# Kernel tuning notes

Measured on AMD Instinct MI355X. Metric: run time of the kernel, lower is better.

The kernel has to match this reference:

```python
import jax, jax.numpy as jnp
import numpy as np

D_MODEL = 1024
HEAD_SIZE = 128
SCALE = float(np.sqrt(HEAD_SIZE))


def setup_inputs() -> dict:
    key = jax.random.key(0)
    kx, kq, kk, kv = jax.random.split(key, 4)
    B, T = 4, 4096
    x = jax.random.normal(kx, (B, T, D_MODEL), dtype=jnp.float32)
    # torch nn.Linear(d_model, head_size, bias=False) weight: [head_size, d_model]
    s = 1.0 / np.sqrt(D_MODEL)
    Wq = jax.random.uniform(kq, (HEAD_SIZE, D_MODEL), jnp.float32, -s, s)
    Wk = jax.random.uniform(kk, (HEAD_SIZE, D_MODEL), jnp.float32, -s, s)
    Wv = jax.random.uniform(kv, (HEAD_SIZE, D_MODEL), jnp.float32, -s, s)
    return {"x": x, "Wq": Wq, "Wk": Wk, "Wv": Wv}


def reference(x, Wq, Wk, Wv):
    B, T, C = x.shape
    q = jnp.einsum('btc,hc->bth', x, Wq)  # [B,T,hs]
    k = jnp.einsum('btc,hc->bth', x, Wk)
    v = jnp.einsum('btc,hc->bth', x, Wv)
    scores = jnp.einsum('bth,bsh->bts', q, k) / SCALE  # [B,T,T]
    causal = jnp.tril(jnp.ones((T, T), dtype=bool))
    scores = jnp.where(causal, scores, -jnp.inf)
    attn = jax.nn.softmax(scores, axis=-1)
    # dropout p=0.0 -> identity
    return jnp.einsum('bts,bsh->bth', attn, v)
```

## Files before the change

### kernel.cpp

```cpp
#include <hip/hip_runtime.h>


typedef __attribute__((ext_vector_type(8))) short short8;
typedef __attribute__((ext_vector_type(8))) unsigned short ushort8;
typedef __attribute__((ext_vector_type(4))) unsigned short ushort4v;
typedef __attribute__((ext_vector_type(4))) float f32x4;
typedef __attribute__((ext_vector_type(16))) float f32x16;
typedef __attribute__((ext_vector_type(4))) int int4v;
typedef unsigned int u32;
typedef unsigned short u16;

#define MFMA32(a, b, c) __builtin_amdgcn_mfma_f32_32x32x16_bf16((a), (b), (c), 0, 0, 0)
#define WAITVM0() asm volatile("s_waitcnt vmcnt(0)" ::: "memory")
#define NEG_INF (-1e30f)

#define CHUNK 10
#define PITEMS 119
#define NITEMS 476

__device__ __forceinline__ void gload16(const void* g, void* l) {
  __builtin_amdgcn_global_load_lds((const __attribute__((address_space(1))) u32*)g,
                                   (__attribute__((address_space(3))) u32*)l, 16, 0, 0);
}

__device__ __forceinline__ u16 f2bf(float f) {
  u32 u = __builtin_bit_cast(u32, f);
  u = u + 0x7FFFu + ((u >> 16) & 1u);
  return (u16)(u >> 16);
}

__device__ __forceinline__ u32 cvtpk(float lo, float hi) {
  u32 r;
  asm("v_cvt_pk_bf16_f32 %0, %1, %2" : "=v"(r) : "v"(lo), "v"(hi));
  return r;
}

__global__ __launch_bounds__(256) void wconv_kernel(const float* __restrict__ Wq,
                                                    const float* __restrict__ Wk,
                                                    const float* __restrict__ Wv,
                                                    u16* __restrict__ Wb) {
  int g = (blockIdx.x * 256 + threadIdx.x) * 8;
  const float* src;
  if (g < 131072)      src = Wq + g;
  else if (g < 262144) src = Wk + (g - 131072);
  else                 src = Wv + (g - 262144);
  float4 a = *(const float4*)src;
  float4 b = *(const float4*)(src + 4);
  ushort8 o;
  o[0] = f2bf(a.x); o[1] = f2bf(a.y); o[2] = f2bf(a.z); o[3] = f2bf(a.w);
  o[4] = f2bf(b.x); o[5] = f2bf(b.y); o[6] = f2bf(b.z); o[7] = f2bf(b.w);
  *(ushort8*)(Wb + g) = o;
}

#define QK_SCALE 0.127517446f

__global__ __launch_bounds__(512, 2) void qkv_proj_kernel(const float* __restrict__ x,
                                                          const u16* __restrict__ Wb,
                                                          u16* __restrict__ qout,
                                                          u16* __restrict__ kout,
                                                          u16* __restrict__ vtout) {
  __shared__ __align__(16) unsigned char Wlds[2][49152];
  __shared__ __align__(16) unsigned char Xlds[2][8192];
  const int tid = threadIdx.x;
  const int w = tid >> 6;
  const int l = tid & 63;
  const int h = l >> 5, n32 = l & 31;
  const int mh = w >> 2, ng = w & 3;
  const int m0 = (int)blockIdx.x * 64;

  const int xr = tid >> 3, xc = tid & 7;
  const float* xsrc = x + (size_t)(m0 + xr) * 1024 + xc * 8;
  unsigned char* const xw0 = (unsigned char*)Xlds[0] + xr * 128 + ((xc * 16) ^ ((xr & 7) << 4));
  unsigned char* const xw1 = (unsigned char*)Xlds[1] + xr * 128 + ((xc * 16) ^ ((xr & 7) << 4));

  f32x16 acc[3];
#pragma unroll
  for (int j = 0; j < 3; ++j)
#pragma unroll
    for (int r = 0; r < 16; ++r) acc[j][r] = 0.f;

#define STAGE_W(buf, ks)                                                       \
  {                                                                            \
    _Pragma("unroll") for (int c = 0; c < 6; ++c) {                            \
      int L = c * 512 + tid;                                                   \
      int row = L >> 3, chp = L & 7;                                           \
      int gch = chp ^ (row & 7);                                               \
      gload16((const char*)Wb + row * 2048 + (ks) * 128 + gch * 16,            \
              (unsigned char*)Wlds[buf] + c * 8192 + w * 1024);                \
    }                                                                          \
  }

  float4 xa = *(const float4*)(xsrc);
  float4 xb = *(const float4*)(xsrc + 4);
  STAGE_W(0, 0);

  const int am = mh * 32 + n32;
  const int asw = (am & 7) << 4;
  int cur = 0;

  for (int ks = 0; ks < 16; ++ks) {
    int4v xv;
    xv[0] = (int)cvtpk(xa.x, xa.y);
    xv[1] = (int)cvtpk(xa.z, xa.w);
    xv[2] = (int)cvtpk(xb.x, xb.y);
    xv[3] = (int)cvtpk(xb.z, xb.w);
    *(int4v*)(cur ? xw1 : xw0) = xv;
    __syncthreads();
    if (ks < 15) {
      xa = *(const float4*)(xsrc + (ks + 1) * 64);
      xb = *(const float4*)(xsrc + (ks + 1) * 64 + 4);
      STAGE_W(cur ^ 1, ks + 1);
    }
    const char* xb0 = (const char*)Xlds[cur];
    const char* wb0 = (const char*)Wlds[cur];
    __builtin_amdgcn_s_setprio(1);
#pragma unroll
    for (int k16 = 0; k16 < 4; ++k16) {
      short8 a = *(const short8*)(xb0 + am * 128 + ((k16 * 32 + h * 16) ^ asw));
#pragma unroll
      for (int j = 0; j < 3; ++j) {
        int nrow = (ng * 3 + j) * 32 + n32;
        short8 b = *(const short8*)(wb0 + nrow * 128 +
                                    ((k16 * 32 + h * 16) ^ ((nrow & 7) << 4)));
        acc[j] = MFMA32(a, b, acc[j]);
      }
    }
    __builtin_amdgcn_s_setprio(0);
    cur ^= 1;
  }
#undef STAGE_W

  const int m0e = m0 + mh * 32;
#pragma unroll
  for (int j = 0; j < 3; ++j) {
    int ti = ng * 3 + j;
    int gcol = ti * 32 + n32;
    if (ti < 4) {
#pragma unroll
      for (int r = 0; r < 16; ++r) {
        int row = m0e + (r & 3) + 8 * (r >> 2) + 4 * h;
        qout[(size_t)row * 128 + gcol] = f2bf(acc[j][r] * QK_SCALE);
      }
    } else if (ti < 8) {
#pragma unroll
      for (int r = 0; r < 16; ++r) {
        int row = m0e + (r & 3) + 8 * (r >> 2) + 4 * h;
        kout[(size_t)row * 128 + (gcol - 128)] = f2bf(acc[j][r]);
      }
    } else {
      int d = gcol - 256;
#pragma unroll
      for (int rq = 0; rq < 4; ++rq) {
        int t0 = m0e + rq * 8 + 4 * h;
        ushort4v o4;
#pragma unroll
        for (int i = 0; i < 4; ++i) o4[i] = f2bf(acc[j][rq * 4 + i]);
        *(ushort4v*)&vtout[(size_t)((t0 >> 12) * 128 + d) * 4096 + (t0 & 4095)] = o4;
      }
    }
  }
}

template <bool SPLIT>
__global__ __launch_bounds__(256, 2) void attn_kernel(const u16* __restrict__ qws,
                                                      const u16* __restrict__ kws,
                                                      const u16* __restrict__ vtws,
                                                      float* __restrict__ out,
                                                      float* __restrict__ opart,
                                                      float* __restrict__ mlpart) {
  __shared__ __align__(16) unsigned char Klds[2][16384];
  __shared__ __align__(16) unsigned char Vlds[2][16384];

  const int tid = threadIdx.x;
  const int w = tid >> 6;
  const int l = tid & 63;
  const int h = l >> 5, q32 = l & 31;

  int bi, qt, s_lo, s_hi, item;
  if constexpr (SPLIT) {
    item = (int)blockIdx.x;
    bi = item / PITEMS;
    int r = item - bi * PITEMS;
    int base = 0;
    qt = 0;
    while (true) {
      int cnt = (qt + 5) / 5;
      if (r < base + cnt) { break; }
      base += cnt;
      ++qt;
    }
    int cc = r - base;
    int nsteps = 2 * qt + 2;
    s_lo = cc * CHUNK;
    s_hi = (s_lo + CHUNK < nsteps) ? s_lo + CHUNK : nsteps;
  } else {
    item = 0;
    int tb = (int)blockIdx.x;
    bi = tb & 3;
    qt = 31 - (tb >> 2);
    s_lo = 0;
    s_hi = 2 * qt + 2;
  }

  const int q0w = qt * 128 + w * 32;
  const int qg = q0w + q32;
  const int grow = bi * 4096 + qg;
  const int ql = w * 32 + q32;

  short8 qf[8];
  const u16* qp = qws + (size_t)grow * 128 + h * 8;
#pragma unroll
  for (int ks = 0; ks < 8; ++ks) qf[ks] = *(const short8*)(qp + ks * 16);

  f32x16 ot[4];
#pragma unroll
  for (int dt = 0; dt < 4; ++dt)
#pragma unroll
    for (int r = 0; r < 16; ++r) ot[dt][r] = 0.f;
  float mreg = NEG_INF, lsum = 0.f;

  const char* kbatch = (const char*)kws + (size_t)bi * 4096 * 256;
  const char* vbatch = (const char*)vtws + (size_t)bi * 128 * 8192;

#define STAGE_KV(buf, kv0)                                                     \
  {                                                                            \
    _Pragma("unroll") for (int c = 0; c < 4; ++c) {                            \
      int L = c * 256 + tid;                                                   \
      int row = L >> 4, chp = L & 15;                                          \
      int gch = chp ^ (row & 7);                                               \
      gload16(kbatch + (size_t)((kv0) + row) * 256 + gch * 16,                 \
              (unsigned char*)Klds[buf] + c * 4096 + w * 1024);                \
    }                                                                          \
    _Pragma("unroll") for (int c = 0; c < 4; ++c) {                            \
      int L = c * 256 + tid;                                                   \
      int row = L >> 3, chp = L & 7;                                           \
      int gch = chp ^ (row & 7);                                               \
      gload16(vbatch + (size_t)row * 8192 + (size_t)(kv0) * 2 + gch * 16,      \
              (unsigned char*)Vlds[buf] + c * 4096 + w * 1024);                \
    }                                                                          \
  }

  STAGE_KV(0, s_lo * 64);
  int cur = 0;

  for (int s = s_lo; s < s_hi; ++s) {
    WAITVM0();
    __builtin_amdgcn_s_barrier();
    __builtin_amdgcn_sched_barrier(0);
    if (s + 1 < s_hi) STAGE_KV(cur ^ 1, (s + 1) * 64);
    const int kv0 = s * 64;
    const bool active = (kv0 <= q0w + 31);

    if (active) {
      f32x16 st0, st1;
#pragma unroll
      for (int r = 0; r < 16; ++r) { st0[r] = 0.f; st1[r] = 0.f; }
      const char* Kb = (const char*)Klds[cur];
      const int sw = (q32 & 7) << 4;
      __builtin_amdgcn_s_setprio(1);
#pragma unroll
      for (int ks = 0; ks < 8; ++ks) {
        int coff = ks * 32 + h * 16;
        short8 a0 = *(const short8*)(Kb + q32 * 256 + (coff ^ sw));
        st0 = MFMA32(a0, qf[ks], st0);
        short8 a1 = *(const short8*)(Kb + (32 + q32) * 256 + (coff ^ sw));
        st1 = MFMA32(a1, qf[ks], st1);
      }
      __builtin_amdgcn_s_setprio(0);

      if (kv0 + 63 > q0w) {
#pragma unroll
        for (int r = 0; r < 16; ++r) {
          int kvr = kv0 + (r & 3) + 8 * (r >> 2) + 4 * h;
          if (kvr > qg) st0[r] = NEG_INF;
          if (kvr + 32 > qg) st1[r] = NEG_INF;
        }
      }

      float tmax = st0[0];
#pragma unroll
      for (int r = 1; r < 16; ++r) tmax = fmaxf(tmax, st0[r]);
#pragma unroll
      for (int r = 0; r < 16; ++r) tmax = fmaxf(tmax, st1[r]);
      tmax = fmaxf(tmax, __shfl_xor(tmax, 32));
      if (!__all(tmax <= mreg + 8.0f)) {
        float mnew = fmaxf(mreg, tmax);
        float alpha = exp2f(mreg - mnew);
        lsum *= alpha;
#pragma unroll
        for (int dt = 0; dt < 4; ++dt)
#pragma unroll
          for (int r = 0; r < 16; ++r) ot[dt][r] *= alpha;
        mreg = mnew;
      }
      float rs = 0.f;
#pragma unroll
      for (int r = 0; r < 16; ++r) { st0[r] = exp2f(st0[r] - mreg); rs += st0[r]; }
#pragma unroll
      for (int r = 0; r < 16; ++r) { st1[r] = exp2f(st1[r] - mreg); rs += st1[r]; }
      rs += __shfl_xor(rs, 32);
      lsum += rs;

      const char* Vb = (const char*)Vlds[cur];
      __builtin_amdgcn_s_setprio(1);
#pragma unroll
      for (int t = 0; t < 4; ++t) {
        const f32x16& stt = (t < 2) ? st0 : st1;
        const int rb = (t & 1) * 8;
        u32 A0 = cvtpk(stt[rb + 0], stt[rb + 1]);
        u32 C0 = cvtpk(stt[rb + 2], stt[rb + 3]);
        u32 B0 = cvtpk(stt[rb + 4], stt[rb + 5]);
        u32 D0 = cvtpk(stt[rb + 6], stt[rb + 7]);
        u32 Ax = (u32)__shfl_xor((int)A0, 32);
        u32 Bx = (u32)__shfl_xor((int)B0, 32);
        u32 Cx = (u32)__shfl_xor((int)C0, 32);
        u32 Dx = (u32)__shfl_xor((int)D0, 32);
        int4v pbv;
        pbv[0] = (int)(h ? Bx : A0);
        pbv[1] = (int)(h ? Dx : C0);
        pbv[2] = (int)(h ? B0 : Ax);
        pbv[3] = (int)(h ? D0 : Cx);
        short8 pb = __builtin_bit_cast(short8, pbv);
#pragma unroll
        for (int dt = 0; dt < 4; ++dt) {
          int row = dt * 32 + q32;
          short8 va = *(const short8*)(Vb + row * 128 + ((t * 32 + h * 16) ^ sw));
          ot[dt] = MFMA32(va, pb, ot[dt]);
        }
      }
      __builtin_amdgcn_s_setprio(0);
    }
    cur ^= 1;
  }

  if constexpr (!SPLIT) {
    float inv = 1.0f / lsum;
    float* ob = out + (size_t)grow * 128;
#pragma unroll
    for (int dt = 0; dt < 4; ++dt)
#pragma unroll
      for (int rq = 0; rq < 4; ++rq) {
        f32x4 v4;
#pragma unroll
        for (int i = 0; i < 4; ++i) v4[i] = ot[dt][rq * 4 + i] * inv;
        *(f32x4*)(ob + dt * 32 + rq * 8 + 4 * h) = v4;
      }
  } else {
    float* ob = opart + (size_t)item * 16384 + (size_t)ql * 128;
#pragma unroll
    for (int dt = 0; dt < 4; ++dt)
#pragma unroll
      for (int rq = 0; rq < 4; ++rq) {
        f32x4 v4;
#pragma unroll
        for (int i = 0; i < 4; ++i) v4[i] = ot[dt][rq * 4 + i];
        *(f32x4*)(ob + dt * 32 + rq * 8 + 4 * h) = v4;
      }
    if (h == 0) {
      mlpart[item * 128 + ql] = mreg;
      mlpart[NITEMS * 128 + item * 128 + ql] = lsum;
    }
  }
#undef STAGE_KV
}

__global__ __launch_bounds__(256) void combine_kernel(const float* __restrict__ opart,
                                                      const float* __restrict__ mlpart,
                                                      float* __restrict__ out) {
  int idx = blockIdx.x * 256 + threadIdx.x;
  int row = idx >> 7, d = idx & 127;
  int bi = row >> 12, lrow = row & 4095;
  int qt = lrow >> 7, ql = lrow & 127;
  int base = 0;
#pragma unroll 1
  for (int j = 0; j < qt; ++j) base += (j + 5) / 5;
  int nspl = (qt + 5) / 5;
  int it0 = bi * PITEMS + base;

  float M = NEG_INF;
#pragma unroll 1
  for (int j = 0; j < nspl; ++j)
    M = fmaxf(M, mlpart[(it0 + j) * 128 + ql]);
  float L = 0.f, O = 0.f;
#pragma unroll 1
  for (int j = 0; j < nspl; ++j) {
    float s = exp2f(mlpart[(it0 + j) * 128 + ql] - M);
    L += mlpart[NITEMS * 128 + (it0 + j) * 128 + ql] * s;
    O += opart[(size_t)(it0 + j) * 16384 + (size_t)ql * 128 + d] * s;
  }
  out[(size_t)row * 128 + d] = O / L;
}

extern "C" void kernel_launch(void* const* d_in, const int* in_sizes, int n_in,
                              void* d_out, int out_size, void* d_ws, size_t ws_size,
                              hipStream_t stream) {
  (void)in_sizes; (void)n_in; (void)out_size;
  const float* x  = (const float*)d_in[0];
  const float* Wq = (const float*)d_in[1];
  const float* Wk = (const float*)d_in[2];
  const float* Wv = (const float*)d_in[3];
  float* out = (float*)d_out;
  char* ws = (char*)d_ws;
  u16* qws  = (u16*)(ws);
  u16* kws  = (u16*)(ws + (4u << 20));
  u16* vtws = (u16*)(ws + (8u << 20));
  u16* Wb   = (u16*)(ws + (12u << 20));
  float* opart  = (float*)(ws + (13u << 20));
  float* mlpart = (float*)(ws + (47u << 20));

  wconv_kernel<<<dim3(192), dim3(256), 0, stream>>>(Wq, Wk, Wv, Wb);
  qkv_proj_kernel<<<dim3(256), dim3(512), 0, stream>>>(x, Wb, qws, kws, vtws);
  if (ws_size >= ((size_t)48 << 20)) {
    attn_kernel<true><<<dim3(NITEMS), dim3(256), 0, stream>>>(qws, kws, vtws, nullptr, opart, mlpart);
    combine_kernel<<<dim3(8192), dim3(256), 0, stream>>>(opart, mlpart, out);
  } else {
    attn_kernel<false><<<dim3(128), dim3(256), 0, stream>>>(qws, kws, vtws, out, nullptr, nullptr);
  }
}
```

Measured before the change: 92.62 us.

## Retile QKV projection, triple-buffer weights, split K/V staging, and rebalance attention chunks

The QKV projection moves to 32-row tiles with 256 threads and a K-step of 32. Weights are triple-buffered, waits use partial vmcnt, and Q/K outputs are staged through LDS for coalesced 16-byte stores. The attention kernel single-buffers V and loads it in a separate phase overlapped with QK/softmax, which cuts LDS so occupancy can rise to 3 blocks per CU. It also uses smaller split chunks (8) with more work items and a strided block-to-item mapping. These changes aim to improve overlap and load balance, at the cost of extra barriers per step and more partial results for the combine pass.

```diff
diff --git a/kernel.cpp b/kernel.cpp
--- a/kernel.cpp
+++ b/kernel.cpp
@@ -7,16 +7,19 @@
 typedef __attribute__((ext_vector_type(4))) float f32x4;
 typedef __attribute__((ext_vector_type(16))) float f32x16;
 typedef __attribute__((ext_vector_type(4))) int int4v;
+typedef __attribute__((ext_vector_type(2))) unsigned int u32x2;
 typedef unsigned int u32;
 typedef unsigned short u16;
 
 #define MFMA32(a, b, c) __builtin_amdgcn_mfma_f32_32x32x16_bf16((a), (b), (c), 0, 0, 0)
-#define WAITVM0() asm volatile("s_waitcnt vmcnt(0)" ::: "memory")
+#define WAITVM(n) asm volatile("s_waitcnt vmcnt(" #n ")" ::: "memory")
+#define WAITLGKM0() asm volatile("s_waitcnt lgkmcnt(0)" ::: "memory")
+#define SCHEDB() __builtin_amdgcn_sched_barrier(0)
 #define NEG_INF (-1e30f)
 
-#define CHUNK 10
-#define PITEMS 119
-#define NITEMS 476
+#define CHUNK 8
+#define PITEMS 144
+#define NITEMS 576
 
 __device__ __forceinline__ void gload16(const void* g, void* l) {
   __builtin_amdgcn_global_load_lds((const __attribute__((address_space(1))) u32*)g,
@@ -54,24 +57,22 @@
 
 #define QK_SCALE 0.127517446f
 
-__global__ __launch_bounds__(512, 2) void qkv_proj_kernel(const float* __restrict__ x,
+__global__ __launch_bounds__(256, 2) void qkv_proj_kernel(const float* __restrict__ x,
                                                           const u16* __restrict__ Wb,
                                                           u16* __restrict__ qout,
                                                           u16* __restrict__ kout,
                                                           u16* __restrict__ vtout) {
-  __shared__ __align__(16) unsigned char Wlds[2][49152];
-  __shared__ __align__(16) unsigned char Xlds[2][8192];
+  __shared__ __align__(16) unsigned char Wlds[3][24576];
+  __shared__ __align__(16) unsigned char Xlds[2][2048];
   const int tid = threadIdx.x;
   const int w = tid >> 6;
   const int l = tid & 63;
   const int h = l >> 5, n32 = l & 31;
-  const int mh = w >> 2, ng = w & 3;
-  const int m0 = (int)blockIdx.x * 64;
+  const int m0 = (int)blockIdx.x * 32;
 
   const int xr = tid >> 3, xc = tid & 7;
-  const float* xsrc = x + (size_t)(m0 + xr) * 1024 + xc * 8;
-  unsigned char* const xw0 = (unsigned char*)Xlds[0] + xr * 128 + ((xc * 16) ^ ((xr & 7) << 4));
-  unsigned char* const xw1 = (unsigned char*)Xlds[1] + xr * 128 + ((xc * 16) ^ ((xr & 7) << 4));
+  const float* xsrc = x + (size_t)(m0 + xr) * 1024 + xc * 4;
+  const int xbyte = ((((xc >> 1) ^ (xr & 3)) << 4) | ((xc & 1) << 3));
 
   f32x16 acc[3];
 #pragma unroll
@@ -82,76 +83,75 @@
 #define STAGE_W(buf, ks)                                                       \
   {                                                                            \
     _Pragma("unroll") for (int c = 0; c < 6; ++c) {                            \
-      int L = c * 512 + tid;                                                   \
-      int row = L >> 3, chp = L & 7;                                           \
-      int gch = chp ^ (row & 7);                                               \
-      gload16((const char*)Wb + row * 2048 + (ks) * 128 + gch * 16,            \
-              (unsigned char*)Wlds[buf] + c * 8192 + w * 1024);                \
+      int L = c * 256 + tid;                                                   \
+      int row = L >> 2, chp = L & 3;                                           \
+      int gch = chp ^ (row & 3);                                               \
+      gload16((const char*)Wb + row * 2048 + (ks) * 64 + gch * 16,             \
+              (unsigned char*)Wlds[buf] + c * 4096 + w * 1024);                \
     }                                                                          \
   }
+#define WRITE_X(buf, v4)                                                       \
+  {                                                                            \
+    u32x2 p;                                                                   \
+    p[0] = cvtpk((v4).x, (v4).y);                                              \
+    p[1] = cvtpk((v4).z, (v4).w);                                              \
+    *(u32x2*)((unsigned char*)Xlds[buf] + xr * 64 + xbyte) = p;                \
+  }
 
   float4 xa = *(const float4*)(xsrc);
-  float4 xb = *(const float4*)(xsrc + 4);
   STAGE_W(0, 0);
-
-  const int am = mh * 32 + n32;
-  const int asw = (am & 7) << 4;
-  int cur = 0;
-
-  for (int ks = 0; ks < 16; ++ks) {
-    int4v xv;
-    xv[0] = (int)cvtpk(xa.x, xa.y);
-    xv[1] = (int)cvtpk(xa.z, xa.w);
-    xv[2] = (int)cvtpk(xb.x, xb.y);
-    xv[3] = (int)cvtpk(xb.z, xb.w);
-    *(int4v*)(cur ? xw1 : xw0) = xv;
-    __syncthreads();
-    if (ks < 15) {
-      xa = *(const float4*)(xsrc + (ks + 1) * 64);
-      xb = *(const float4*)(xsrc + (ks + 1) * 64 + 4);
-      STAGE_W(cur ^ 1, ks + 1);
-    }
-    const char* xb0 = (const char*)Xlds[cur];
-    const char* wb0 = (const char*)Wlds[cur];
+  float4 xb = *(const float4*)(xsrc + 32);
+  STAGE_W(1, 1);
+  WRITE_X(0, xa);
+
+  for (int s = 0; s < 32; ++s) {
+    if (s < 31) { WAITVM(7); } else { WAITVM(0); }
+    WAITLGKM0();
+    __builtin_amdgcn_s_barrier();
+    SCHEDB();
+    if (s < 31) WRITE_X((s + 1) & 1, xb);
+    if (s < 30) {
+      xb = *(const float4*)(xsrc + (s + 2) * 32);
+      STAGE_W((s + 2) % 3, s + 2);
+    }
+    SCHEDB();
+    const char* xb0 = (const char*)Xlds[s & 1];
+    const char* wb0 = (const char*)Wlds[s % 3];
     __builtin_amdgcn_s_setprio(1);
 #pragma unroll
-    for (int k16 = 0; k16 < 4; ++k16) {
-      short8 a = *(const short8*)(xb0 + am * 128 + ((k16 * 32 + h * 16) ^ asw));
+    for (int k16 = 0; k16 < 2; ++k16) {
+      short8 a = *(const short8*)(xb0 + n32 * 64 +
+                                  ((k16 * 32 + h * 16) ^ ((n32 & 3) << 4)));
 #pragma unroll
       for (int j = 0; j < 3; ++j) {
-        int nrow = (ng * 3 + j) * 32 + n32;
-        short8 b = *(const short8*)(wb0 + nrow * 128 +
-                                    ((k16 * 32 + h * 16) ^ ((nrow & 7) << 4)));
+        int nrow = (w * 3 + j) * 32 + n32;
+        short8 b = *(const short8*)(wb0 + nrow * 64 +
+                                    ((k16 * 32 + h * 16) ^ ((nrow & 3) << 4)));
         acc[j] = MFMA32(a, b, acc[j]);
       }
     }
     __builtin_amdgcn_s_setprio(0);
-    cur ^= 1;
   }
 #undef STAGE_W
-
-  const int m0e = m0 + mh * 32;
+#undef WRITE_X
+
+  __syncthreads();
+  u16* cl = (u16*)&Wlds[0][0];
 #pragma unroll
   for (int j = 0; j < 3; ++j) {
-    int ti = ng * 3 + j;
-    int gcol = ti * 32 + n32;
-    if (ti < 4) {
+    int ti = w * 3 + j;
+    if (ti < 8) {
+      float sc = (ti < 4) ? QK_SCALE : 1.0f;
 #pragma unroll
       for (int r = 0; r < 16; ++r) {
-        int row = m0e + (r & 3) + 8 * (r >> 2) + 4 * h;
-        qout[(size_t)row * 128 + gcol] = f2bf(acc[j][r] * QK_SCALE);
-      }
-    } else if (ti < 8) {
-#pragma unroll
-      for (int r = 0; r < 16; ++r) {
-        int row = m0e + (r & 3) + 8 * (r >> 2) + 4 * h;
-        kout[(size_t)row * 128 + (gcol - 128)] = f2bf(acc[j][r]);
+        int mm = (r & 3) + 8 * (r >> 2) + 4 * h;
+        cl[mm * 256 + ti * 32 + n32] = f2bf(acc[j][r] * sc);
       }
     } else {
-      int d = gcol - 256;
+      int d = (ti - 8) * 32 + n32;
 #pragma unroll
       for (int rq = 0; rq < 4; ++rq) {
-        int t0 = m0e + rq * 8 + 4 * h;
+        int t0 = m0 + rq * 8 + 4 * h;
         ushort4v o4;
 #pragma unroll
         for (int i = 0; i < 4; ++i) o4[i] = f2bf(acc[j][rq * 4 + i]);
@@ -159,17 +159,29 @@
       }
     }
   }
+  __syncthreads();
+  {
+    int row = tid >> 3;
+    int col0 = (tid & 7) * 32;
+#pragma unroll
+    for (int c = 0; c < 4; ++c) {
+      int col = col0 + c * 8;
+      ushort8 v8 = *(const ushort8*)(cl + row * 256 + col);
+      if (col < 128) *(ushort8*)&qout[(size_t)(m0 + row) * 128 + col] = v8;
+      else           *(ushort8*)&kout[(size_t)(m0 + row) * 128 + (col - 128)] = v8;
+    }
+  }
 }
 
 template <bool SPLIT>
-__global__ __launch_bounds__(256, 2) void attn_kernel(const u16* __restrict__ qws,
+__global__ __launch_bounds__(256, 3) void attn_kernel(const u16* __restrict__ qws,
                                                       const u16* __restrict__ kws,
                                                       const u16* __restrict__ vtws,
                                                       float* __restrict__ out,
                                                       float* __restrict__ opart,
                                                       float* __restrict__ mlpart) {
   __shared__ __align__(16) unsigned char Klds[2][16384];
-  __shared__ __align__(16) unsigned char Vlds[2][16384];
+  __shared__ __align__(16) unsigned char Vlds[16384];
 
   const int tid = threadIdx.x;
   const int w = tid >> 6;
@@ -178,14 +190,15 @@
 
   int bi, qt, s_lo, s_hi, item;
   if constexpr (SPLIT) {
-    item = (int)blockIdx.x;
+    int bx = (int)blockIdx.x;
+    item = (bx & 7) * 72 + (bx >> 3);
     bi = item / PITEMS;
     int r = item - bi * PITEMS;
     int base = 0;
     qt = 0;
     while (true) {
-      int cnt = (qt + 5) / 5;
-      if (r < base + cnt) { break; }
+      int cnt = (qt + 4) >> 2;
+      if (r < base + cnt) break;
       base += cnt;
       ++qt;
     }
@@ -222,7 +235,7 @@
   const char* kbatch = (const char*)kws + (size_t)bi * 4096 * 256;
   const char* vbatch = (const char*)vtws + (size_t)bi * 128 * 8192;
 
-#define STAGE_KV(buf, kv0)                                                     \
+#define STAGE_K(buf, kv0)                                                      \
   {                                                                            \
     _Pragma("unroll") for (int c = 0; c < 4; ++c) {                            \
       int L = c * 256 + tid;                                                   \
@@ -231,28 +244,36 @@
       gload16(kbatch + (size_t)((kv0) + row) * 256 + gch * 16,                 \
               (unsigned char*)Klds[buf] + c * 4096 + w * 1024);                \
     }                                                                          \
+  }
+#define STAGE_V(kv0)                                                           \
+  {                                                                            \
     _Pragma("unroll") for (int c = 0; c < 4; ++c) {                            \
       int L = c * 256 + tid;                                                   \
       int row = L >> 3, chp = L & 7;                                           \
       int gch = chp ^ (row & 7);                                               \
       gload16(vbatch + (size_t)row * 8192 + (size_t)(kv0) * 2 + gch * 16,      \
-              (unsigned char*)Vlds[buf] + c * 4096 + w * 1024);                \
+              (unsigned char*)Vlds + c * 4096 + w * 1024);                     \
     }                                                                          \
   }
 
-  STAGE_KV(0, s_lo * 64);
+  STAGE_K(0, s_lo * 64);
+  SCHEDB();
+  STAGE_V(s_lo * 64);
+  SCHEDB();
   int cur = 0;
 
   for (int s = s_lo; s < s_hi; ++s) {
-    WAITVM0();
+    const bool more = (s + 1 < s_hi);
+    WAITVM(4);
     __builtin_amdgcn_s_barrier();
-    __builtin_amdgcn_sched_barrier(0);
-    if (s + 1 < s_hi) STAGE_KV(cur ^ 1, (s + 1) * 64);
+    SCHEDB();
+    if (more) STAGE_K(cur ^ 1, (s + 1) * 64);
+    SCHEDB();
     const int kv0 = s * 64;
     const bool active = (kv0 <= q0w + 31);
 
+    f32x16 st0, st1;
     if (active) {
-      f32x16 st0, st1;
 #pragma unroll
       for (int r = 0; r < 16; ++r) { st0[r] = 0.f; st1[r] = 0.f; }
       const char* Kb = (const char*)Klds[cur];
@@ -300,8 +321,15 @@
       for (int r = 0; r < 16; ++r) { st1[r] = exp2f(st1[r] - mreg); rs += st1[r]; }
       rs += __shfl_xor(rs, 32);
       lsum += rs;
-
-      const char* Vb = (const char*)Vlds[cur];
+    }
+
+    if (more) { WAITVM(4); } else { WAITVM(0); }
+    __builtin_amdgcn_s_barrier();
+    SCHEDB();
+
+    if (active) {
+      const char* Vb = (const char*)Vlds;
+      const int sw = (q32 & 7) << 4;
       __builtin_amdgcn_s_setprio(1);
 #pragma unroll
       for (int t = 0; t < 4; ++t) {
@@ -330,6 +358,13 @@
       }
       __builtin_amdgcn_s_setprio(0);
     }
+
+    if (more) {
+      __builtin_amdgcn_s_barrier();
+      SCHEDB();
+      STAGE_V((s + 1) * 64);
+      SCHEDB();
+    }
     cur ^= 1;
   }
 
@@ -361,7 +396,8 @@
       mlpart[NITEMS * 128 + item * 128 + ql] = lsum;
     }
   }
-#undef STAGE_KV
+#undef STAGE_K
+#undef STAGE_V
 }
 
 __global__ __launch_bounds__(256) void combine_kernel(const float* __restrict__ opart,
@@ -373,8 +409,8 @@
   int qt = lrow >> 7, ql = lrow & 127;
   int base = 0;
 #pragma unroll 1
-  for (int j = 0; j < qt; ++j) base += (j + 5) / 5;
-  int nspl = (qt + 5) / 5;
+  for (int j = 0; j < qt; ++j) base += (j + 4) >> 2;
+  int nspl = (qt + 4) >> 2;
   int it0 = bi * PITEMS + base;
 
   float M = NEG_INF;
@@ -406,11 +442,11 @@
   u16* vtws = (u16*)(ws + (8u << 20));
   u16* Wb   = (u16*)(ws + (12u << 20));
   float* opart  = (float*)(ws + (13u << 20));
-  float* mlpart = (float*)(ws + (47u << 20));
+  float* mlpart = (float*)(ws + (50u << 20));
 
   wconv_kernel<<<dim3(192), dim3(256), 0, stream>>>(Wq, Wk, Wv, Wb);
-  qkv_proj_kernel<<<dim3(256), dim3(512), 0, stream>>>(x, Wb, qws, kws, vtws);
-  if (ws_size >= ((size_t)48 << 20)) {
+  qkv_proj_kernel<<<dim3(512), dim3(256), 0, stream>>>(x, Wb, qws, kws, vtws);
+  if (ws_size >= ((size_t)52 << 20)) {
     attn_kernel<true><<<dim3(NITEMS), dim3(256), 0, stream>>>(qws, kws, vtws, nullptr, opart, mlpart);
     combine_kernel<<<dim3(8192), dim3(256), 0, stream>>>(opart, mlpart, out);
   } else {
```

Result: slower. 115.0 us (+24.1%).
